# Kernel optimization log

Hardware: AMD Instinct MI355X
Metric: run time of the kernel (lower is better)

The kernel has to match this reference:

```python
import jax, jax.numpy as jnp
import numpy as np

N_HARM_XYZ = 6
N_HARM_DIR = 4
HIDDEN_XYZ = 256
HIDDEN_DIR = 128
EMB_XYZ = N_HARM_XYZ * 2 * 3 + 3  # 39
EMB_DIR = N_HARM_DIR * 2 * 3 + 3  # 27


def harmonic_embedding(x, n_harmonics):
    # x: [..., 3] -> [..., n_harmonics*2*3 + 3]
    freqs = 2.0 ** jnp.arange(n_harmonics, dtype=x.dtype)  # logspace, omega0=1
    emb = (x[..., None] * freqs).reshape(*x.shape[:-1], -1)  # [..., 3*n_harm]
    return jnp.concatenate([jnp.sin(emb), jnp.cos(emb), x], axis=-1)


def setup_inputs() -> dict:
    key = jax.random.key(0)
    ks = jax.random.split(key, 32)
    R, P = 2048, 64
    inp = {
        'sample_points': jax.random.normal(ks[0], (R, P, 3), dtype=jnp.float32),
        'directions': jax.random.normal(ks[1], (R, 3), dtype=jnp.float32),
    }
    # trunk layer dims (skip concat before layer 5; last layer outputs hidden+1)
    dims_in = [EMB_XYZ, HIDDEN_XYZ, HIDDEN_XYZ, HIDDEN_XYZ, HIDDEN_XYZ,
               HIDDEN_XYZ + EMB_XYZ, HIDDEN_XYZ, HIDDEN_XYZ]
    dims_out = [HIDDEN_XYZ] * 7 + [HIDDEN_XYZ + 1]
    for i, (di, do) in enumerate(zip(dims_in, dims_out)):
        s = 1.0 / np.sqrt(di)
        inp[f'W{i}'] = jax.random.uniform(ks[2 + 2 * i], (di, do), jnp.float32, -s, s)
        inp[f'b{i}'] = jax.random.uniform(ks[3 + 2 * i], (do,), jnp.float32, -s, s)
    s = 1.0 / np.sqrt(HIDDEN_XYZ + EMB_DIR)
    inp['Wc'] = jax.random.uniform(ks[20], (HIDDEN_XYZ + EMB_DIR, HIDDEN_DIR), jnp.float32, -s, s)
    inp['bc'] = jax.random.uniform(ks[21], (HIDDEN_DIR,), jnp.float32, -s, s)
    s = 1.0 / np.sqrt(HIDDEN_DIR)
    inp['Wo'] = jax.random.uniform(ks[22], (HIDDEN_DIR, 3), jnp.float32, -s, s)
    inp['bo'] = jax.random.uniform(ks[23], (3,), jnp.float32, -s, s)
    return inp


def nerf_forward(sample_points, directions,
                 W0, b0, W1, b1, W2, b2, W3, b3, W4, b4, W5, b5, W6, b6, W7, b7,
                 Wc, bc, Wo, bo):
    R, P, _ = sample_points.shape
    pts = sample_points.reshape(-1, 3)              # [N, 3]
    e = harmonic_embedding(pts, N_HARM_XYZ)         # [N, 39]
    h = e
    # seq0: layers 0-4, ReLU after each
    for W, b in ((W0, b0), (W1, b1), (W2, b2), (W3, b3), (W4, b4)):
        h = jax.nn.relu(h @ W + b)
    # skip concat with xyz embedding, then seq1: layers 5-7 (no ReLU after last)
    h = jnp.concatenate([h, e], axis=-1)            # [N, 295]
    h = jax.nn.relu(h @ W5 + b5)
    h = jax.nn.relu(h @ W6 + b6)
    h = h @ W7 + b7                                  # [N, 257]
    sigma = jax.nn.relu(h[:, 0]).reshape(R, P, 1)
    dirs = jnp.broadcast_to(directions[:, None, :], (R, P, 3)).reshape(-1, 3)
    d = harmonic_embedding(dirs, N_HARM_DIR)         # [N, 27]
    c = jnp.concatenate([h[:, 1:], d], axis=-1)      # [N, 283]
    c = jax.nn.relu(c @ Wc + bc)
    color = jax.nn.sigmoid(c @ Wo + bo).reshape(R, P, 3)
    return color, sigma


def reference(sample_points, directions,
              W0, b0, W1, b1, W2, b2, W3, b3, W4, b4, W5, b5, W6, b6, W7, b7,
              Wc, bc, Wo, bo):
    # returns (feature, density) matching the torch dict values
    return nerf_forward(sample_points, directions,
                        W0, b0, W1, b1, W2, b2, W3, b3, W4, b4, W5, b5, W6, b6, W7, b7,
                        Wc, bc, Wo, bo)
```

## Files before the change

### kernel.cpp

```cpp
#include <hip/hip_runtime.h>

typedef __attribute__((ext_vector_type(8))) __bf16 bf16x8;
typedef __attribute__((ext_vector_type(4))) float float4_;
typedef __attribute__((ext_vector_type(4))) unsigned short ushort4_;
typedef __attribute__((ext_vector_type(8))) unsigned short ushort8_;

#define OFF_W0T 0
#define OFF_W1T 16384
#define OFF_W2T 81920
#define OFF_W3T 147456
#define OFF_W4T 212992
#define OFF_W5T 278528
#define OFF_W6T 360448
#define OFF_W7T 425984
#define OFF_WCT 491520
#define BF16_TOTAL 524288
#define WSF_BYTE_OFF (BF16_TOTAL * 2)

__device__ __forceinline__ unsigned short f2b(float v) {
  union { float f; unsigned u; } a; a.f = v;
  unsigned r = a.u + 0x7fffu + ((a.u >> 16) & 1u);
  return (unsigned short)(r >> 16);
}

__device__ __forceinline__ ushort4_ pack4(float4_ v) {
#if __has_builtin(__builtin_amdgcn_cvt_pk_bf16_f32)
  auto p0 = __builtin_amdgcn_cvt_pk_bf16_f32(v.x, v.y);
  auto p1 = __builtin_amdgcn_cvt_pk_bf16_f32(v.z, v.w);
  union { decltype(p0) p; unsigned u; } u0, u1;
  u0.p = p0; u1.p = p1;
  ushort4_ r;
  r.x = (unsigned short)(u0.u & 0xffffu); r.y = (unsigned short)(u0.u >> 16);
  r.z = (unsigned short)(u1.u & 0xffffu); r.w = (unsigned short)(u1.u >> 16);
  return r;
#else
  ushort4_ r; r.x = f2b(v.x); r.y = f2b(v.y); r.z = f2b(v.z); r.w = f2b(v.w);
  return r;
#endif
}

__global__ __launch_bounds__(256) void prep_kernel(
    const float* __restrict__ W0, const float* __restrict__ W1,
    const float* __restrict__ W2, const float* __restrict__ W3,
    const float* __restrict__ W4, const float* __restrict__ W5,
    const float* __restrict__ W6, const float* __restrict__ W7,
    const float* __restrict__ Wc, const float* __restrict__ b7,
    unsigned short* __restrict__ wsb, float* __restrict__ wsf)
{
  int i = blockIdx.x * 256 + threadIdx.x;
  const float* src; int rs, K, Kp, n, k2; unsigned short* base;
  if (i < 8192)        { int t = i;          n = t & 255; k2 = t >> 8; src = W0; rs = 256; K = 39;  Kp = 64;  base = wsb + OFF_W0T; }
  else if (i < 139264) { int t = i - 8192;   int l = t >> 15; t &= 32767;
                         n = t & 255; k2 = t >> 8;
                         src = (l == 0) ? W1 : (l == 1) ? W2 : (l == 2) ? W3 : W4;
                         rs = 256; K = 256; Kp = 256; base = wsb + OFF_W1T + l * 65536; }
  else if (i < 180224) { int t = i - 139264; n = t & 255; k2 = t >> 8; src = W5;     rs = 256; K = 295; Kp = 320; base = wsb + OFF_W5T; }
  else if (i < 212992) { int t = i - 180224; n = t & 255; k2 = t >> 8; src = W6;     rs = 256; K = 256; Kp = 256; base = wsb + OFF_W6T; }
  else if (i < 245760) { int t = i - 212992; n = t & 255; k2 = t >> 8; src = W7 + 1; rs = 257; K = 256; Kp = 256; base = wsb + OFF_W7T; }
  else if (i < 262144) { int t = i - 245760; n = t & 127; k2 = t >> 7; src = Wc;     rs = 128; K = 256; Kp = 256; base = wsb + OFF_WCT; }
  else if (i < 262400) { int k = i - 262144; wsf[k] = W7[k * 257]; return; }
  else if (i < 262656) { int k = i - 262400; wsf[256 + k] = b7[k + 1]; return; }
  else return;
  const int k = k2 * 2;
  const float v0 = (k     < K) ? src[k * rs + n]       : 0.f;
  const float v1 = (k + 1 < K) ? src[(k + 1) * rs + n] : 0.f;
  const int off = (((n >> 4) * (Kp >> 5)) + (k >> 5)) * 512
                + ((k >> 3) & 3) * 128 + (n & 15) * 8 + (k & 7);
  const unsigned val = (unsigned)f2b(v0) | ((unsigned)f2b(v1) << 16);
  *(unsigned*)(base + off) = val;
}

template<int KS1, int KS2, bool RELU>
__device__ __forceinline__ void layer_mm(
    const unsigned short* src1, const unsigned short* src2,
    const unsigned short* __restrict__ wT,
    const float* bias, unsigned short* dst, int lane, int wave)
{
  constexpr int KT = KS1 + KS2;
  const int c = lane & 15, q = lane >> 4;
  const int nt0 = wave * 2, n0 = wave * 32;
  const unsigned short* wl = wT + lane * 8;

  float4_ bv0 = *(const float4_*)(bias + n0 + q * 4);
  float4_ bv1 = *(const float4_*)(bias + n0 + 16 + q * 4);
  float4_ acc[4][2];
#pragma unroll
  for (int mi = 0; mi < 4; ++mi) { acc[mi][0] = bv0; acc[mi][1] = bv1; }

  bf16x8 aC0 = *(const bf16x8*)(wl + (nt0 * KT) * 512);
  bf16x8 aC1 = *(const bf16x8*)(wl + ((nt0 + 1) * KT) * 512);
#pragma unroll
  for (int ks = 0; ks < KT; ++ks) {
    bf16x8 aN0, aN1;
    if (ks + 1 < KT) {
      aN0 = *(const bf16x8*)(wl + (nt0 * KT + ks + 1) * 512);
      aN1 = *(const bf16x8*)(wl + ((nt0 + 1) * KT + ks + 1) * 512);
    }
    const unsigned short* bsrc = (ks < KS1) ? src1 + (ks * 4) * 512
                                            : src2 + ((ks - KS1) * 4) * 512;
    bf16x8 bfr[4];
#pragma unroll
    for (int mi = 0; mi < 4; ++mi)
      bfr[mi] = *(const bf16x8*)(bsrc + mi * 512 + lane * 8);
#pragma unroll
    for (int mi = 0; mi < 4; ++mi) {
      acc[mi][0] = __builtin_amdgcn_mfma_f32_16x16x32_bf16(aC0, bfr[mi], acc[mi][0], 0, 0, 0);
      acc[mi][1] = __builtin_amdgcn_mfma_f32_16x16x32_bf16(aC1, bfr[mi], acc[mi][1], 0, 0, 0);
    }
    if (ks + 1 < KT) { aC0 = aN0; aC1 = aN1; }
  }
#pragma unroll
  for (int ni = 0; ni < 2; ++ni) {
    const int base = n0 + ni * 16 + q * 4;
#pragma unroll
    for (int mi = 0; mi < 4; ++mi) {
      float4_ v = acc[mi][ni];
      if (RELU) {
        v.x = fmaxf(v.x, 0.f); v.y = fmaxf(v.y, 0.f);
        v.z = fmaxf(v.z, 0.f); v.w = fmaxf(v.w, 0.f);
      }
      const int addr = ((base >> 5) * 4 + mi) * 512
                     + ((base >> 3) & 3) * 128 + c * 8 + (base & 7);
      *(ushort4_*)(dst + addr) = pack4(v);
    }
  }
}

__global__ __launch_bounds__(512, 4) void nerf_kernel(
    const float* __restrict__ pts, const float* __restrict__ dirs,
    const float* __restrict__ b0, const float* __restrict__ b1,
    const float* __restrict__ b2, const float* __restrict__ b3,
    const float* __restrict__ b4, const float* __restrict__ b5,
    const float* __restrict__ b6, const float* __restrict__ b7,
    const float* __restrict__ Wc, const float* __restrict__ bc,
    const float* __restrict__ Wo, const float* __restrict__ bo,
    const unsigned short* __restrict__ wsb, const float* __restrict__ wsf,
    float* __restrict__ out)
{
  __shared__ __align__(16) unsigned short sA[32 * 512];
  __shared__ __align__(16) unsigned short sB[40 * 512];
  __shared__ float s_dvec[27];
  __shared__ float s_biasc[128];

  const int ray = blockIdx.x;
  const int t = threadIdx.x;
  const int lane = t & 63;
  const int wave = t >> 6;
  unsigned short* sE = sB + 32 * 512;

  {
    const int m = t >> 3, s8 = t & 7;
    const float* pb = pts + (ray * 64 + m) * 3;
    const float x0 = pb[0], x1 = pb[1], x2 = pb[2];
    ushort8_ ev;
#pragma unroll
    for (int j = 0; j < 8; ++j) {
      const int cc = s8 * 8 + j;
      float v = 0.f;
      if (cc < 18) {
        const float xx = (cc < 6) ? x0 : (cc < 12) ? x1 : x2;
        v = sinf(xx * (float)(1 << (cc % 6)));
      } else if (cc < 36) {
        const int c2 = cc - 18;
        const float xx = (c2 < 6) ? x0 : (c2 < 12) ? x1 : x2;
        v = cosf(xx * (float)(1 << (c2 % 6)));
      } else if (cc == 36) v = x0;
      else if (cc == 37) v = x1;
      else if (cc == 38) v = x2;
      ev[j] = f2b(v);
    }
    *(ushort8_*)(sE + ((s8 >> 2) * 4 + (m >> 4)) * 512 + (s8 & 3) * 128 + (m & 15) * 8) = ev;
  }
  if (t < 27) {
    const float* db = dirs + ray * 3;
    float v;
    if (t < 12) v = sinf(db[t >> 2] * (float)(1 << (t & 3)));
    else if (t < 24) { const int j = t - 12; v = cosf(db[j >> 2] * (float)(1 << (j & 3))); }
    else v = db[t - 24];
    s_dvec[t] = v;
  }
  __syncthreads();
  if (t < 128) {
    float s = bc[t];
#pragma unroll
    for (int j = 0; j < 27; ++j) s += s_dvec[j] * Wc[(256 + j) * 128 + t];
    s_biasc[t] = s;
  }

  layer_mm<2, 0, true >(sE, nullptr, wsb + OFF_W0T, b0, sA, lane, wave); __syncthreads();
  layer_mm<8, 0, true >(sA, nullptr, wsb + OFF_W1T, b1, sB, lane, wave); __syncthreads();
  layer_mm<8, 0, true >(sB, nullptr, wsb + OFF_W2T, b2, sA, lane, wave); __syncthreads();
  layer_mm<8, 0, true >(sA, nullptr, wsb + OFF_W3T, b3, sB, lane, wave); __syncthreads();
  layer_mm<8, 0, true >(sB, nullptr, wsb + OFF_W4T, b4, sA, lane, wave); __syncthreads();
  layer_mm<8, 2, true >(sA, sE,      wsb + OFF_W5T, b5, sB, lane, wave); __syncthreads();
  layer_mm<8, 0, true >(sB, nullptr, wsb + OFF_W6T, b6, sA, lane, wave); __syncthreads();

  {
    const int m = t >> 3, q8 = t & 7;
    const unsigned short* pbase = sA + (q8 * 4 + (m >> 4)) * 512 + (m & 15) * 8;
    const float* w = wsf + q8 * 32;
    float s = 0.f;
#pragma unroll
    for (int i8 = 0; i8 < 4; ++i8) {
      bf16x8 hv = *(const bf16x8*)(pbase + i8 * 128);
#pragma unroll
      for (int j = 0; j < 8; ++j) s += (float)hv[j] * w[i8 * 8 + j];
    }
    s += __shfl_xor(s, 1); s += __shfl_xor(s, 2); s += __shfl_xor(s, 4);
    if (q8 == 0) out[393216 + ray * 64 + m] = fmaxf(s + b7[0], 0.f);
  }

  layer_mm<8, 0, false>(sA, nullptr, wsb + OFF_W7T, wsf + 256, sB, lane, wave); __syncthreads();
  if (wave < 4)
    layer_mm<8, 0, true>(sB, nullptr, wsb + OFF_WCT, s_biasc, sA, lane, wave);
  __syncthreads();

  {
    const int m = t >> 3, q8 = t & 7;
    float s0 = 0.f, s1 = 0.f, s2 = 0.f;
#pragma unroll
    for (int i2 = 0; i2 < 2; ++i2) {
      const int kb = q8 * 16 + i2 * 8;
      bf16x8 cv = *(const bf16x8*)(sA + ((kb >> 5) * 4 + (m >> 4)) * 512
                                      + ((kb >> 3) & 3) * 128 + (m & 15) * 8);
#pragma unroll
      for (int j = 0; j < 8; ++j) {
        const float cc = (float)cv[j];
        const float* w = Wo + (kb + j) * 3;
        s0 += cc * w[0]; s1 += cc * w[1]; s2 += cc * w[2];
      }
    }
    s0 += __shfl_xor(s0, 1); s0 += __shfl_xor(s0, 2); s0 += __shfl_xor(s0, 4);
    s1 += __shfl_xor(s1, 1); s1 += __shfl_xor(s1, 2); s1 += __shfl_xor(s1, 4);
    s2 += __shfl_xor(s2, 1); s2 += __shfl_xor(s2, 2); s2 += __shfl_xor(s2, 4);
    if (q8 == 0) {
      float* oc = out + (ray * 64 + m) * 3;
      oc[0] = 1.f / (1.f + __expf(-(s0 + bo[0])));
      oc[1] = 1.f / (1.f + __expf(-(s1 + bo[1])));
      oc[2] = 1.f / (1.f + __expf(-(s2 + bo[2])));
    }
  }
}

extern "C" void kernel_launch(void* const* d_in, const int* in_sizes, int n_in,
                              void* d_out, int out_size, void* d_ws, size_t ws_size,
                              hipStream_t stream)
{
  const float* pts  = (const float*)d_in[0];
  const float* dirs = (const float*)d_in[1];
  const float* W0 = (const float*)d_in[2];   const float* b0 = (const float*)d_in[3];
  const float* W1 = (const float*)d_in[4];   const float* b1 = (const float*)d_in[5];
  const float* W2 = (const float*)d_in[6];   const float* b2 = (const float*)d_in[7];
  const float* W3 = (const float*)d_in[8];   const float* b3 = (const float*)d_in[9];
  const float* W4 = (const float*)d_in[10];  const float* b4 = (const float*)d_in[11];
  const float* W5 = (const float*)d_in[12];  const float* b5 = (const float*)d_in[13];
  const float* W6 = (const float*)d_in[14];  const float* b6 = (const float*)d_in[15];
  const float* W7 = (const float*)d_in[16];  const float* b7 = (const float*)d_in[17];
  const float* Wc = (const float*)d_in[18];  const float* bc = (const float*)d_in[19];
  const float* Wo = (const float*)d_in[20];  const float* bo = (const float*)d_in[21];

  unsigned short* wsb = (unsigned short*)d_ws;
  float* wsf = (float*)((char*)d_ws + WSF_BYTE_OFF);

  prep_kernel<<<1026, 256, 0, stream>>>(W0, W1, W2, W3, W4, W5, W6, W7, Wc, b7, wsb, wsf);
  nerf_kernel<<<2048, 512, 0, stream>>>(pts, dirs, b0, b1, b2, b3, b4, b5, b6, b7,
                                        Wc, bc, Wo, bo, wsb, wsf, (float*)d_out);
}
```

Baseline: 246.2 us.

## Use 4 waves with 64-column tiles per wave and K-major weight layout

```diff
diff --git a/kernel.cpp b/kernel.cpp
--- a/kernel.cpp
+++ b/kernel.cpp
@@ -48,29 +48,29 @@
     unsigned short* __restrict__ wsb, float* __restrict__ wsf)
 {
   int i = blockIdx.x * 256 + threadIdx.x;
-  const float* src; int rs, K, Kp, n, k2; unsigned short* base;
-  if (i < 8192)        { int t = i;          n = t & 255; k2 = t >> 8; src = W0; rs = 256; K = 39;  Kp = 64;  base = wsb + OFF_W0T; }
+  const float* src; int rs, K, n, k2, nt16; unsigned short* base;
+  if (i < 8192)        { int t = i;          n = t & 255; k2 = t >> 8; src = W0; rs = 256; K = 39;  nt16 = 16; base = wsb + OFF_W0T; }
   else if (i < 139264) { int t = i - 8192;   int l = t >> 15; t &= 32767;
                          n = t & 255; k2 = t >> 8;
                          src = (l == 0) ? W1 : (l == 1) ? W2 : (l == 2) ? W3 : W4;
-                         rs = 256; K = 256; Kp = 256; base = wsb + OFF_W1T + l * 65536; }
-  else if (i < 180224) { int t = i - 139264; n = t & 255; k2 = t >> 8; src = W5;     rs = 256; K = 295; Kp = 320; base = wsb + OFF_W5T; }
-  else if (i < 212992) { int t = i - 180224; n = t & 255; k2 = t >> 8; src = W6;     rs = 256; K = 256; Kp = 256; base = wsb + OFF_W6T; }
-  else if (i < 245760) { int t = i - 212992; n = t & 255; k2 = t >> 8; src = W7 + 1; rs = 257; K = 256; Kp = 256; base = wsb + OFF_W7T; }
-  else if (i < 262144) { int t = i - 245760; n = t & 127; k2 = t >> 7; src = Wc;     rs = 128; K = 256; Kp = 256; base = wsb + OFF_WCT; }
+                         rs = 256; K = 256; nt16 = 16; base = wsb + OFF_W1T + l * 65536; }
+  else if (i < 180224) { int t = i - 139264; n = t & 255; k2 = t >> 8; src = W5;     rs = 256; K = 295; nt16 = 16; base = wsb + OFF_W5T; }
+  else if (i < 212992) { int t = i - 180224; n = t & 255; k2 = t >> 8; src = W6;     rs = 256; K = 256; nt16 = 16; base = wsb + OFF_W6T; }
+  else if (i < 245760) { int t = i - 212992; n = t & 255; k2 = t >> 8; src = W7 + 1; rs = 257; K = 256; nt16 = 16; base = wsb + OFF_W7T; }
+  else if (i < 262144) { int t = i - 245760; n = t & 127; k2 = t >> 7; src = Wc;     rs = 128; K = 256; nt16 = 8;  base = wsb + OFF_WCT; }
   else if (i < 262400) { int k = i - 262144; wsf[k] = W7[k * 257]; return; }
   else if (i < 262656) { int k = i - 262400; wsf[256 + k] = b7[k + 1]; return; }
   else return;
   const int k = k2 * 2;
   const float v0 = (k     < K) ? src[k * rs + n]       : 0.f;
   const float v1 = (k + 1 < K) ? src[(k + 1) * rs + n] : 0.f;
-  const int off = (((n >> 4) * (Kp >> 5)) + (k >> 5)) * 512
+  const int off = ((k >> 5) * nt16 + (n >> 4)) * 512
                 + ((k >> 3) & 3) * 128 + (n & 15) * 8 + (k & 7);
   const unsigned val = (unsigned)f2b(v0) | ((unsigned)f2b(v1) << 16);
   *(unsigned*)(base + off) = val;
 }
 
-template<int KS1, int KS2, bool RELU>
+template<int NT, int NTB, int KS1, int KS2, bool RELU>
 __device__ __forceinline__ void layer_mm(
     const unsigned short* src1, const unsigned short* src2,
     const unsigned short* __restrict__ wT,
@@ -78,23 +78,27 @@
 {
   constexpr int KT = KS1 + KS2;
   const int c = lane & 15, q = lane >> 4;
-  const int nt0 = wave * 2, n0 = wave * 32;
-  const unsigned short* wl = wT + lane * 8;
-
-  float4_ bv0 = *(const float4_*)(bias + n0 + q * 4);
-  float4_ bv1 = *(const float4_*)(bias + n0 + 16 + q * 4);
-  float4_ acc[4][2];
-#pragma unroll
-  for (int mi = 0; mi < 4; ++mi) { acc[mi][0] = bv0; acc[mi][1] = bv1; }
-
-  bf16x8 aC0 = *(const bf16x8*)(wl + (nt0 * KT) * 512);
-  bf16x8 aC1 = *(const bf16x8*)(wl + ((nt0 + 1) * KT) * 512);
+  const int n0 = wave * (NT * 16);
+  const unsigned short* wl = wT + (wave * NT) * 512 + lane * 8;
+
+  float4_ acc[4][NT];
+#pragma unroll
+  for (int ni = 0; ni < NT; ++ni) {
+    float4_ bv = *(const float4_*)(bias + n0 + ni * 16 + q * 4);
+#pragma unroll
+    for (int mi = 0; mi < 4; ++mi) acc[mi][ni] = bv;
+  }
+
+  bf16x8 aC[NT], aN[NT];
+#pragma unroll
+  for (int ni = 0; ni < NT; ++ni)
+    aC[ni] = *(const bf16x8*)(wl + ni * 512);
 #pragma unroll
   for (int ks = 0; ks < KT; ++ks) {
-    bf16x8 aN0, aN1;
     if (ks + 1 < KT) {
-      aN0 = *(const bf16x8*)(wl + (nt0 * KT + ks + 1) * 512);
-      aN1 = *(const bf16x8*)(wl + ((nt0 + 1) * KT + ks + 1) * 512);
+#pragma unroll
+      for (int ni = 0; ni < NT; ++ni)
+        aN[ni] = *(const bf16x8*)(wl + ((ks + 1) * NTB + ni) * 512);
     }
     const unsigned short* bsrc = (ks < KS1) ? src1 + (ks * 4) * 512
                                             : src2 + ((ks - KS1) * 4) * 512;
@@ -103,14 +107,17 @@
     for (int mi = 0; mi < 4; ++mi)
       bfr[mi] = *(const bf16x8*)(bsrc + mi * 512 + lane * 8);
 #pragma unroll
-    for (int mi = 0; mi < 4; ++mi) {
-      acc[mi][0] = __builtin_amdgcn_mfma_f32_16x16x32_bf16(aC0, bfr[mi], acc[mi][0], 0, 0, 0);
-      acc[mi][1] = __builtin_amdgcn_mfma_f32_16x16x32_bf16(aC1, bfr[mi], acc[mi][1], 0, 0, 0);
-    }
-    if (ks + 1 < KT) { aC0 = aN0; aC1 = aN1; }
-  }
-#pragma unroll
-  for (int ni = 0; ni < 2; ++ni) {
+    for (int ni = 0; ni < NT; ++ni)
+#pragma unroll
+      for (int mi = 0; mi < 4; ++mi)
+        acc[mi][ni] = __builtin_amdgcn_mfma_f32_16x16x32_bf16(aC[ni], bfr[mi], acc[mi][ni], 0, 0, 0);
+    if (ks + 1 < KT) {
+#pragma unroll
+      for (int ni = 0; ni < NT; ++ni) aC[ni] = aN[ni];
+    }
+  }
+#pragma unroll
+  for (int ni = 0; ni < NT; ++ni) {
     const int base = n0 + ni * 16 + q * 4;
 #pragma unroll
     for (int mi = 0; mi < 4; ++mi) {
@@ -126,7 +133,7 @@
   }
 }
 
-__global__ __launch_bounds__(512, 4) void nerf_kernel(
+__global__ __launch_bounds__(256, 2) void nerf_kernel(
     const float* __restrict__ pts, const float* __restrict__ dirs,
     const float* __restrict__ b0, const float* __restrict__ b1,
     const float* __restrict__ b2, const float* __restrict__ b3,
@@ -149,27 +156,32 @@
   unsigned short* sE = sB + 32 * 512;
 
   {
-    const int m = t >> 3, s8 = t & 7;
+    const int m = t >> 2, s4 = t & 3;
     const float* pb = pts + (ray * 64 + m) * 3;
     const float x0 = pb[0], x1 = pb[1], x2 = pb[2];
-    ushort8_ ev;
-#pragma unroll
-    for (int j = 0; j < 8; ++j) {
-      const int cc = s8 * 8 + j;
-      float v = 0.f;
-      if (cc < 18) {
-        const float xx = (cc < 6) ? x0 : (cc < 12) ? x1 : x2;
-        v = sinf(xx * (float)(1 << (cc % 6)));
-      } else if (cc < 36) {
-        const int c2 = cc - 18;
-        const float xx = (c2 < 6) ? x0 : (c2 < 12) ? x1 : x2;
-        v = cosf(xx * (float)(1 << (c2 % 6)));
-      } else if (cc == 36) v = x0;
-      else if (cc == 37) v = x1;
-      else if (cc == 38) v = x2;
-      ev[j] = f2b(v);
-    }
-    *(ushort8_*)(sE + ((s8 >> 2) * 4 + (m >> 4)) * 512 + (s8 & 3) * 128 + (m & 15) * 8) = ev;
+#pragma unroll
+    for (int h = 0; h < 2; ++h) {
+      ushort8_ ev;
+#pragma unroll
+      for (int j = 0; j < 8; ++j) {
+        const int cc = s4 * 16 + h * 8 + j;
+        float v = 0.f;
+        if (cc < 18) {
+          const float xx = (cc < 6) ? x0 : (cc < 12) ? x1 : x2;
+          v = sinf(xx * (float)(1 << (cc % 6)));
+        } else if (cc < 36) {
+          const int c2 = cc - 18;
+          const float xx = (c2 < 6) ? x0 : (c2 < 12) ? x1 : x2;
+          v = cosf(xx * (float)(1 << (c2 % 6)));
+        } else if (cc == 36) v = x0;
+        else if (cc == 37) v = x1;
+        else if (cc == 38) v = x2;
+        ev[j] = f2b(v);
+      }
+      const int cc0 = s4 * 16 + h * 8;
+      *(ushort8_*)(sE + ((cc0 >> 5) * 4 + (m >> 4)) * 512
+                      + ((cc0 >> 3) & 3) * 128 + (m & 15) * 8) = ev;
+    }
   }
   if (t < 27) {
     const float* db = dirs + ray * 3;
@@ -187,40 +199,39 @@
     s_biasc[t] = s;
   }
 
-  layer_mm<2, 0, true >(sE, nullptr, wsb + OFF_W0T, b0, sA, lane, wave); __syncthreads();
-  layer_mm<8, 0, true >(sA, nullptr, wsb + OFF_W1T, b1, sB, lane, wave); __syncthreads();
-  layer_mm<8, 0, true >(sB, nullptr, wsb + OFF_W2T, b2, sA, lane, wave); __syncthreads();
-  layer_mm<8, 0, true >(sA, nullptr, wsb + OFF_W3T, b3, sB, lane, wave); __syncthreads();
-  layer_mm<8, 0, true >(sB, nullptr, wsb + OFF_W4T, b4, sA, lane, wave); __syncthreads();
-  layer_mm<8, 2, true >(sA, sE,      wsb + OFF_W5T, b5, sB, lane, wave); __syncthreads();
-  layer_mm<8, 0, true >(sB, nullptr, wsb + OFF_W6T, b6, sA, lane, wave); __syncthreads();
+  layer_mm<4, 16, 2,  0, true >(sE, nullptr, wsb + OFF_W0T, b0, sA, lane, wave); __syncthreads();
+  layer_mm<4, 16, 8,  0, true >(sA, nullptr, wsb + OFF_W1T, b1, sB, lane, wave); __syncthreads();
+  layer_mm<4, 16, 8,  0, true >(sB, nullptr, wsb + OFF_W2T, b2, sA, lane, wave); __syncthreads();
+  layer_mm<4, 16, 8,  0, true >(sA, nullptr, wsb + OFF_W3T, b3, sB, lane, wave); __syncthreads();
+  layer_mm<4, 16, 8,  0, true >(sB, nullptr, wsb + OFF_W4T, b4, sA, lane, wave); __syncthreads();
+  layer_mm<4, 16, 8,  2, true >(sA, sE,      wsb + OFF_W5T, b5, sB, lane, wave); __syncthreads();
+  layer_mm<4, 16, 8,  0, true >(sB, nullptr, wsb + OFF_W6T, b6, sA, lane, wave); __syncthreads();
 
   {
-    const int m = t >> 3, q8 = t & 7;
-    const unsigned short* pbase = sA + (q8 * 4 + (m >> 4)) * 512 + (m & 15) * 8;
-    const float* w = wsf + q8 * 32;
+    const int m = t >> 2, q4 = t & 3;
     float s = 0.f;
 #pragma unroll
+    for (int i8 = 0; i8 < 8; ++i8) {
+      const int kb = q4 * 64 + i8 * 8;
+      bf16x8 hv = *(const bf16x8*)(sA + ((kb >> 5) * 4 + (m >> 4)) * 512
+                                      + ((kb >> 3) & 3) * 128 + (m & 15) * 8);
+      const float* w = wsf + kb;
+#pragma unroll
+      for (int j = 0; j < 8; ++j) s += (float)hv[j] * w[j];
+    }
+    s += __shfl_xor(s, 1); s += __shfl_xor(s, 2);
+    if (q4 == 0) out[393216 + ray * 64 + m] = fmaxf(s + b7[0], 0.f);
+  }
+
+  layer_mm<4, 16, 8, 0, false>(sA, nullptr, wsb + OFF_W7T, wsf + 256, sB, lane, wave); __syncthreads();
+  layer_mm<2, 8,  8, 0, true >(sB, nullptr, wsb + OFF_WCT, s_biasc, sA, lane, wave); __syncthreads();
+
+  {
+    const int m = t >> 2, q4 = t & 3;
+    float s0 = 0.f, s1 = 0.f, s2 = 0.f;
+#pragma unroll
     for (int i8 = 0; i8 < 4; ++i8) {
-      bf16x8 hv = *(const bf16x8*)(pbase + i8 * 128);
-#pragma unroll
-      for (int j = 0; j < 8; ++j) s += (float)hv[j] * w[i8 * 8 + j];
-    }
-    s += __shfl_xor(s, 1); s += __shfl_xor(s, 2); s += __shfl_xor(s, 4);
-    if (q8 == 0) out[393216 + ray * 64 + m] = fmaxf(s + b7[0], 0.f);
-  }
-
-  layer_mm<8, 0, false>(sA, nullptr, wsb + OFF_W7T, wsf + 256, sB, lane, wave); __syncthreads();
-  if (wave < 4)
-    layer_mm<8, 0, true>(sB, nullptr, wsb + OFF_WCT, s_biasc, sA, lane, wave);
-  __syncthreads();
-
-  {
-    const int m = t >> 3, q8 = t & 7;
-    float s0 = 0.f, s1 = 0.f, s2 = 0.f;
-#pragma unroll
-    for (int i2 = 0; i2 < 2; ++i2) {
-      const int kb = q8 * 16 + i2 * 8;
+      const int kb = q4 * 32 + i8 * 8;
       bf16x8 cv = *(const bf16x8*)(sA + ((kb >> 5) * 4 + (m >> 4)) * 512
                                       + ((kb >> 3) & 3) * 128 + (m & 15) * 8);
 #pragma unroll
@@ -230,10 +241,10 @@
         s0 += cc * w[0]; s1 += cc * w[1]; s2 += cc * w[2];
       }
     }
-    s0 += __shfl_xor(s0, 1); s0 += __shfl_xor(s0, 2); s0 += __shfl_xor(s0, 4);
-    s1 += __shfl_xor(s1, 1); s1 += __shfl_xor(s1, 2); s1 += __shfl_xor(s1, 4);
-    s2 += __shfl_xor(s2, 1); s2 += __shfl_xor(s2, 2); s2 += __shfl_xor(s2, 4);
-    if (q8 == 0) {
+    s0 += __shfl_xor(s0, 1); s0 += __shfl_xor(s0, 2);
+    s1 += __shfl_xor(s1, 1); s1 += __shfl_xor(s1, 2);
+    s2 += __shfl_xor(s2, 1); s2 += __shfl_xor(s2, 2);
+    if (q4 == 0) {
       float* oc = out + (ray * 64 + m) * 3;
       oc[0] = 1.f / (1.f + __expf(-(s0 + bo[0])));
       oc[1] = 1.f / (1.f + __expf(-(s1 + bo[1])));
@@ -263,6 +274,6 @@
   float* wsf = (float*)((char*)d_ws + WSF_BYTE_OFF);
 
   prep_kernel<<<1026, 256, 0, stream>>>(W0, W1, W2, W3, W4, W5, W6, W7, Wc, b7, wsb, wsf);
-  nerf_kernel<<<2048, 512, 0, stream>>>(pts, dirs, b0, b1, b2, b3, b4, b5, b6, b7,
+  nerf_kernel<<<2048, 256, 0, stream>>>(pts, dirs, b0, b1, b2, b3, b4, b5, b6, b7,
                                         Wc, bc, Wo, bo, wsb, wsf, (float*)d_out);
 }
```

Result: slower. 287.1 us (+16.6%).
